# Performance work log

Measured on AMD Instinct MI355X. Metric: run time of the kernel, lower is better.

Reference implementation:

```python
import jax, jax.numpy as jnp
import numpy as np

C = 128        # in_channels
N = 80000      # nodes per type (user, item)
E = 1000000    # edges per relation
L = 400000     # link labels


def _evolve_gcn(x_src, edge_index, n_dst, p, W0, Wih, Whh, bih, bhh):
    """EvolveGCNH layer: TopK pooling -> 1-step GRU weight evolution -> GCN."""
    # TopK pooling: score = x @ p / ||p||, keep top C nodes, gate by tanh(score)
    score = x_src @ p / (jnp.linalg.norm(p) + 1e-16)          # [N_src]
    top_vals, top_idx = jax.lax.top_k(score, x_src.shape[1])   # k = C
    X_tilde = x_src[top_idx] * jnp.tanh(top_vals)[:, None]     # [C, C]
    # One GRU step: 'batch' dim = C rows of X_tilde, hidden = current weight W0
    gi = X_tilde @ Wih.T + bih                                 # [C, 3C]
    gh = W0 @ Whh.T + bhh                                      # [C, 3C]
    i_r, i_z, i_n = jnp.split(gi, 3, axis=1)
    h_r, h_z, h_n = jnp.split(gh, 3, axis=1)
    r = jax.nn.sigmoid(i_r + h_r)
    z = jax.nn.sigmoid(i_z + h_z)
    n = jnp.tanh(i_n + r * h_n)
    W = (1.0 - z) * n + z * W0                                 # evolved weight [C, C]
    # GCN propagation with symmetric degree norm, no self loops
    xw = x_src @ W                                             # [N_src, C]
    row, col = edge_index[0], edge_index[1]
    ones = jnp.ones(row.shape[0], dtype=xw.dtype)
    deg_src = jax.ops.segment_sum(ones, row, num_segments=x_src.shape[0])
    deg_dst = jax.ops.segment_sum(ones, col, num_segments=n_dst)
    inv_s = jnp.where(deg_src > 0, jax.lax.rsqrt(jnp.maximum(deg_src, 1.0)), 0.0)
    inv_d = jnp.where(deg_dst > 0, jax.lax.rsqrt(jnp.maximum(deg_dst, 1.0)), 0.0)
    norm = inv_s[row] * inv_d[col]                             # [E]
    return jax.ops.segment_sum(xw[row] * norm[:, None], col, num_segments=n_dst)


def setup_inputs() -> dict:
    key = jax.random.key(0)
    ks = jax.random.split(key, 20)
    f = lambda i, shape, s: jax.random.normal(ks[i], shape, dtype=jnp.float32) * s
    s_w = 1.0 / np.sqrt(C)
    return {
        "x_user": f(0, (N, C), 1.0),
        "x_item": f(1, (N, C), 1.0),
        "edge_ui": jax.random.randint(ks[2], (2, E), 0, N),
        "edge_iu": jax.random.randint(ks[3], (2, E), 0, N),
        "edge_label_index": jax.random.randint(ks[4], (2, L), 0, N),
        "p_ui": f(5, (C,), s_w),
        "W0_ui": f(6, (C, C), s_w),
        "Wih_ui": f(7, (3 * C, C), s_w),
        "Whh_ui": f(8, (3 * C, C), s_w),
        "bih_ui": f(9, (3 * C,), s_w),
        "bhh_ui": f(10, (3 * C,), s_w),
        "p_iu": f(11, (C,), s_w),
        "W0_iu": f(12, (C, C), s_w),
        "Wih_iu": f(13, (3 * C, C), s_w),
        "Whh_iu": f(14, (3 * C, C), s_w),
        "bih_iu": f(15, (3 * C,), s_w),
        "bhh_iu": f(16, (3 * C,), s_w),
        "W_post": f(17, (C, 2), s_w),
        "b_post": f(18, (2,), s_w),
    }


def reference(x_user, x_item, edge_ui, edge_iu, edge_label_index,
              p_ui, W0_ui, Wih_ui, Whh_ui, bih_ui, bhh_ui,
              p_iu, W0_iu, Wih_iu, Whh_iu, bih_iu, bhh_iu,
              W_post, b_post):
    # HeteroConv: one EvolveGCNH per relation, outputs grouped by dst node type
    h_item = jax.nn.relu(_evolve_gcn(x_user, edge_ui, x_item.shape[0],
                                     p_ui, W0_ui, Wih_ui, Whh_ui, bih_ui, bhh_ui))
    h_user = jax.nn.relu(_evolve_gcn(x_item, edge_iu, x_user.shape[0],
                                     p_iu, W0_iu, Wih_iu, Whh_iu, bih_iu, bhh_iu))
    # Link scorer: gather endpoints, hadamard, linear(C->2), sum over last dim
    h_src = h_user[edge_label_index[0]]                        # [L, C]
    h_dst = h_item[edge_label_index[1]]                        # [L, C]
    h = (h_src * h_dst) @ W_post + b_post                      # [L, 2]
    return jnp.sum(h, axis=-1)                                 # [L]
```

## Files before the change

kernel.cpp:

```cpp
#include <hip/hip_runtime.h>
#include <hip/hip_fp16.h>

constexpr int KC    = 128;
constexpr int NBLK  = 2048;
constexpr int CAPA  = 1024;
constexpr int CBITS = 10;
constexpr int CSZ   = 1 << CBITS;
constexpr int NBCM  = 192;

using half8   = __attribute__((ext_vector_type(8))) _Float16;
using float4v = __attribute__((ext_vector_type(4))) float;

__device__ __forceinline__ unsigned fkey(float s) {
  unsigned u = __float_as_uint(s);
  return (u & 0x80000000u) ? ~u : (u | 0x80000000u);
}

__global__ __launch_bounds__(256) void m1_cnt_scores(
    const int* __restrict__ eui, const int* __restrict__ eiu,
    unsigned* __restrict__ cnts, int* __restrict__ deg_src,
    const float* __restrict__ xu, const float* __restrict__ xi,
    const float* __restrict__ pu, const float* __restrict__ pi,
    float* __restrict__ scores, unsigned* __restrict__ hist,
    __half* __restrict__ x16,
    int E, int N, int NBC, int chunk) {
  __shared__ unsigned hD[4 * NBCM];
  int t = threadIdx.x;
  if (blockIdx.x < NBLK) {
    int blk = blockIdx.x, w = t >> 6;
    for (int b = t; b < 4 * NBCM; b += 256) hD[b] = 0;
    __syncthreads();
    int lo = blk * chunk, hi = min(2 * E, lo + chunk);
    for (int i = lo + t; i < hi; i += 256) {
      int rel = i >= E;
      const int* e = rel ? eiu : eui;
      int j = i - rel * E;
      atomicAdd(&hD[w * NBCM + ((rel * N + e[E + j]) >> CBITS)], 1u);
      atomicAdd(&deg_src[rel * N + e[j]], 1);
    }
    __syncthreads();
    for (int b = t; b < NBC; b += 256)
      cnts[(size_t)blk * NBC + b] =
          hD[b] + hD[NBCM + b] + hD[2 * NBCM + b] + hD[3 * NBCM + b];
  } else {
    int gw = (blockIdx.x - NBLK) * 8 + (t >> 5);
    if (gw >= 2 * N) return;
    int lane = t & 31;
    int rel = gw >= N;
    int r = gw - rel * N;
    const float* x = rel ? xi : xu;
    const float* p = rel ? pi : pu;
    float4 xv = ((const float4*)(x + (size_t)r * KC))[lane];
    float4 pv = ((const float4*)p)[lane];
    __half2 h0 = __floats2half2_rn(xv.x, xv.y);
    __half2 h1 = __floats2half2_rn(xv.z, xv.w);
    uint2 u; u.x = *(unsigned*)&h0; u.y = *(unsigned*)&h1;
    ((uint2*)(x16 + (size_t)gw * KC))[lane] = u;
    float s = xv.x * pv.x + xv.y * pv.y + xv.z * pv.z + xv.w * pv.w;
#pragma unroll
    for (int off = 16; off; off >>= 1) s += __shfl_down(s, off, 32);
    if (lane == 0) {
      scores[gw] = s;
      atomicAdd(&hist[rel * 65536 + (fkey(s) >> 16)], 1u);
    }
  }
}

__global__ __launch_bounds__(1024) void m2_thresh_scan1(
    const unsigned* __restrict__ cnts, unsigned* __restrict__ sc,
    unsigned* __restrict__ bsum, const unsigned* __restrict__ hist,
    unsigned* __restrict__ ctrl, int NTOT, int NBC) {
  __shared__ __align__(16) unsigned smem[1024 + 64 + 2];
  int t = threadIdx.x;
  if (blockIdx.x < 2) {
    const unsigned* h = hist + blockIdx.x * 65536;
    unsigned* c = ctrl + blockIdx.x * 8;
    unsigned* csum = smem;
    unsigned* bs = smem + 1024;
    unsigned s = 0;
    int hi = 65536 - 64 * t;
    for (int b = hi - 64; b < hi; ++b) s += h[b];
    csum[t] = s;
    __syncthreads();
    for (int off = 1; off < 1024; off <<= 1) {
      unsigned add = (t >= off) ? csum[t - off] : 0;
      __syncthreads();
      csum[t] += add;
      __syncthreads();
    }
    unsigned above = (t == 0) ? 0u : csum[t - 1];
    if (csum[t] >= 128u && above < 128u) { smem[1088] = (unsigned)t; smem[1089] = above; }
    __syncthreads();
    int chi = 65536 - 64 * (int)smem[1088];
    unsigned s_above = smem[1089];
    if (t < 64) bs[t] = h[chi - 1 - t];
    __syncthreads();
    if (t < 64) {
      unsigned v = bs[t], cum = v;
#pragma unroll
      for (int off = 1; off < 64; off <<= 1) {
        unsigned u = __shfl_up(cum, off, 64);
        if (t >= off) cum += u;
      }
      unsigned prev = cum - v;
      if (s_above + cum >= 128u && s_above + prev < 128u)
        c[0] = (unsigned)(chi - 1 - t);
    }
  } else {
    int vb = blockIdx.x - 2;
    unsigned* sh = smem;
    int li = vb * 1024 + t;
    unsigned v = 0;
    if (li < NTOT) {
      int b = li >> 11, blk = li & (NBLK - 1);
      v = cnts[(size_t)blk * NBC + b];
    }
    sh[t] = v; __syncthreads();
    for (int off = 1; off < 1024; off <<= 1) {
      unsigned add = (t >= off) ? sh[t - off] : 0;
      __syncthreads();
      sh[t] += add;
      __syncthreads();
    }
    if (li < NTOT) sc[li] = sh[t] - v;
    if (t == 1023) bsum[vb] = sh[1023];
  }
}

__global__ __launch_bounds__(512) void m3_scan2_compact(
    unsigned* __restrict__ bsum, int nb,
    const float* __restrict__ scores, unsigned* __restrict__ ctrl,
    int* __restrict__ cand_idx, float* __restrict__ cand_val, int N) {
  if (blockIdx.x == 0) {
    __shared__ unsigned sh[512];
    int t = threadIdx.x;
    unsigned v = (t < nb) ? bsum[t] : 0;
    sh[t] = v; __syncthreads();
    for (int off = 1; off < 512; off <<= 1) {
      unsigned add = (t >= off) ? sh[t - off] : 0;
      __syncthreads();
      sh[t] += add;
      __syncthreads();
    }
    if (t < nb) bsum[t] = sh[t] - v;
  } else {
    int i = (blockIdx.x - 1) * 512 + threadIdx.x;
    if (i >= 2 * N) return;
    int rel = i >= N;
    float s = scores[i];
    if ((fkey(s) >> 16) >= ctrl[rel * 8]) {
      unsigned pos = atomicAdd(&ctrl[rel * 8 + 1], 1u);
      if (pos < 2048u) {
        cand_idx[rel * 2048 + pos] = i - rel * N;
        cand_val[rel * 2048 + pos] = s;
      }
    }
  }
}

__global__ __launch_bounds__(256) void m4_topk_part(
    const int* __restrict__ eui, const int* __restrict__ eiu,
    const unsigned* __restrict__ cnts, const unsigned* __restrict__ sc,
    const unsigned* __restrict__ bsum,
    unsigned* __restrict__ recsD,
    const unsigned* __restrict__ ctrl,
    const int* __restrict__ cand_idx, const float* __restrict__ cand_val,
    const float* __restrict__ pu, const float* __restrict__ pi,
    int* __restrict__ top_idx, float* __restrict__ top_tanh,
    int E, int N, int NBC, int chunk) {
  __shared__ __align__(16) char smem[16896];
  int t = threadIdx.x;
  if (blockIdx.x < 2) {
    float* vals = (float*)smem;
    int*   idxs = (int*)(smem + 8192);
    float* red  = (float*)(smem + 16384);
    int rel = blockIdx.x;
    const float* p = rel ? pi : pu;
    int n = (int)ctrl[rel * 8 + 1]; if (n > 2048) n = 2048;
    for (int i = t; i < n; i += 256) {
      vals[i] = cand_val[rel * 2048 + i];
      idxs[i] = cand_idx[rel * 2048 + i];
    }
    if (t < 128) { float pv = p[t]; red[t] = pv * pv; }
    __syncthreads();
    for (int off = 64; off; off >>= 1) {
      if (t < off) red[t] += red[t + off];
      __syncthreads();
    }
    float pn = sqrtf(red[0]) + 1e-16f;
    for (int c = t; c < n; c += 256) {
      float v = vals[c]; int id = idxs[c];
      int rank = 0;
      for (int j = 0; j < n; ++j) {
        float vj = vals[j];
        rank += (vj > v) || (vj == v && idxs[j] < id);
      }
      if (rank < KC) {
        top_idx[rel * KC + rank] = id;
        top_tanh[rel * KC + rank] = tanhf(v / pn);
      }
    }
  } else {
    unsigned* scn    = (unsigned*)smem;
    unsigned* curD   = (unsigned*)(smem + 1024);
    unsigned* deltaD = (unsigned*)(smem + 2048);
    unsigned* stageD = (unsigned*)(smem + 3072);
    unsigned char* bktD = (unsigned char*)(smem + 7168);
    int blk = blockIdx.x - 2;
    unsigned v = (t < NBC) ? cnts[(size_t)blk * NBC + t] : 0;
    scn[t] = v; __syncthreads();
    for (int off = 1; off < 256; off <<= 1) {
      unsigned add = (t >= off) ? scn[t - off] : 0;
      __syncthreads();
      scn[t] += add;
      __syncthreads();
    }
    if (t < NBC) {
      unsigned exc = scn[t] - v;
      curD[t] = exc;
      int li = t * NBLK + blk;
      deltaD[t] = sc[li] + bsum[li >> 10] - exc;
    }
    __syncthreads();
    int lo = blk * chunk, hi = min(2 * E, lo + chunk);
    for (int i = lo + t; i < hi; i += 256) {
      int rel = i >= E;
      const int* e = rel ? eiu : eui;
      int j = i - rel * E;
      int src_g = rel * N + e[j];
      int dst_g = rel * N + e[E + j];
      int bD = dst_g >> CBITS;
      unsigned pD = atomicAdd(&curD[bD], 1u);
      stageD[pD] = (unsigned)src_g | ((unsigned)(dst_g & (CSZ - 1)) << 18);
      bktD[pD] = (unsigned char)bD;
    }
    __syncthreads();
    int cnt = hi - lo;
    for (int j = t; j < cnt; j += 256)
      recsD[deltaD[bktD[j]] + j] = stageD[j];
  }
}

__global__ __launch_bounds__(1024) void m5_refine_gru(
    const unsigned* __restrict__ sc, const unsigned* __restrict__ bsum,
    const unsigned* __restrict__ recsD,
    int* __restrict__ ssrc, int* __restrict__ deg_dst, int* __restrict__ endp,
    const float* __restrict__ xu, const float* __restrict__ xi,
    const int* __restrict__ top_idx, const float* __restrict__ top_tanh,
    const float* __restrict__ W0u, const float* __restrict__ W0i,
    const float* __restrict__ Wihu, const float* __restrict__ Wihi,
    const float* __restrict__ Whhu, const float* __restrict__ Whhi,
    const float* __restrict__ bihu, const float* __restrict__ bihi,
    const float* __restrict__ bhhu, const float* __restrict__ bhhi,
    __half* __restrict__ Wt,
    int E, int NBC, int N2) {
  __shared__ __align__(16) char smem[8256];
  int t = threadIdx.x;
  if ((int)blockIdx.x < NBC) {
    unsigned* hist = (unsigned*)smem;
    unsigned* cur  = (unsigned*)(smem + 4096);
    unsigned* t16  = (unsigned*)(smem + 8192);
    int c = blockIdx.x;
    int liLo = c * NBLK;
    int lo = (int)(sc[liLo] + bsum[liLo >> 10]);
    int hi;
    if (c + 1 < NBC) {
      int liHi = (c + 1) * NBLK;
      hi = (int)(sc[liHi] + bsum[liHi >> 10]);
    } else hi = 2 * E;
    hist[t] = 0;
    __syncthreads();
    for (int j = lo + t; j < hi; j += 1024)
      atomicAdd(&hist[recsD[j] >> 18], 1u);
    __syncthreads();
    unsigned v = hist[t];
    unsigned inc = v;
#pragma unroll
    for (int off = 1; off < 64; off <<= 1) {
      unsigned u = __shfl_up(inc, off, 64);
      if ((t & 63) >= off) inc += u;
    }
    int w = t >> 6;
    if ((t & 63) == 63) t16[w] = inc;
    __syncthreads();
    unsigned wbase = 0;
    for (int j = 0; j < 16; ++j) if (j < w) wbase += t16[j];
    unsigned exc = wbase + inc - v;
    cur[t] = exc;
    int node = c * CSZ + t;
    if (node < N2) {
      deg_dst[node] = (int)v;
      endp[node] = lo + (int)(exc + v);
    }
    __syncthreads();
    for (int j = lo + t; j < hi; j += 1024) {
      unsigned rec = recsD[j];
      unsigned pos = atomicAdd(&cur[rec >> 18], 1u);
      ssrc[lo + (int)pos] = (int)(rec & 0x3FFFFu);
    }
  } else {
    int gb = blockIdx.x - NBC;
    int rel = gb >> 7, c = gb & 127;
    const float* x   = rel ? xi   : xu;
    const float* W0  = rel ? W0i  : W0u;
    const float* Wih = rel ? Wihi : Wihu;
    const float* Whh = rel ? Whhi : Whhu;
    const float* bih = rel ? bihi : bihu;
    const float* bhh = rel ? bhhi : bhhu;
    float* xt = (float*)smem;
    float* w0 = (float*)(smem + 512);
    if (t < KC) {
      xt[t] = x[(size_t)top_idx[rel * KC + c] * KC + t] * top_tanh[rel * KC + c];
      w0[t] = W0[c * KC + t];
    }
    __syncthreads();
    if (t >= KC) return;
    int k = t;
    float gir = bih[k], giz = bih[KC + k], gin = bih[2 * KC + k];
    float ghr = bhh[k], ghz = bhh[KC + k], ghn = bhh[2 * KC + k];
    const float* wr = Wih + (size_t)k * KC;
    const float* wz = Wih + (size_t)(KC + k) * KC;
    const float* wn = Wih + (size_t)(2 * KC + k) * KC;
    const float* vr = Whh + (size_t)k * KC;
    const float* vz = Whh + (size_t)(KC + k) * KC;
    const float* vn = Whh + (size_t)(2 * KC + k) * KC;
    for (int j = 0; j < KC; ++j) {
      float xj = xt[j], hj = w0[j];
      gir += xj * wr[j]; giz += xj * wz[j]; gin += xj * wn[j];
      ghr += hj * vr[j]; ghz += hj * vz[j]; ghn += hj * vn[j];
    }
    float r = 1.f / (1.f + expf(-(gir + ghr)));
    float z = 1.f / (1.f + expf(-(giz + ghz)));
    float nn = tanhf(gin + r * ghn);
    float w = (1.f - z) * nn + z * w0[k];
    Wt[(size_t)rel * KC * KC + (size_t)k * KC + c] = __float2half_rn(w);
  }
}

__global__ __launch_bounds__(256) void k_gemm(const __half* __restrict__ x16,
                                              const __half* __restrict__ Wt,
                                              const int* __restrict__ deg_src,
                                              __half* __restrict__ xw, int N) {
  __shared__ __half Ws[KC * KC];
  __shared__ __half outs[64 * 136];
  int rel = (blockIdx.x * 64) >= N;
  int t = threadIdx.x;
  const uint4* wg = (const uint4*)(Wt + (size_t)rel * KC * KC);
#pragma unroll
  for (int i = 0; i < 8; ++i)
    ((uint4*)Ws)[t + 256 * i] = wg[t + 256 * i];
  __syncthreads();
  int wid = t >> 6, lane = t & 63;
  int l15 = lane & 15, quad = lane >> 4;
  int row0 = blockIdx.x * 64 + wid * 16;
  half8 a[4];
  const __half* xrow = x16 + (size_t)(row0 + l15) * KC + quad * 8;
#pragma unroll
  for (int ks = 0; ks < 4; ++ks) a[ks] = *(const half8*)(xrow + ks * 32);
  float4v acc[8];
#pragma unroll
  for (int nt = 0; nt < 8; ++nt) {
    acc[nt] = (float4v){0.f, 0.f, 0.f, 0.f};
#pragma unroll
    for (int ks = 0; ks < 4; ++ks) {
      half8 b = *(const half8*)&Ws[(nt * 16 + l15) * KC + ks * 32 + quad * 8];
      acc[nt] = __builtin_amdgcn_mfma_f32_16x16x32_f16(a[ks], b, acc[nt], 0, 0, 0);
    }
  }
  float scv[4];
#pragma unroll
  for (int r = 0; r < 4; ++r) {
    int dg = deg_src[row0 + quad * 4 + r];
    scv[r] = dg > 0 ? rsqrtf((float)dg) : 0.f;
  }
  __half* ob = outs + (size_t)wid * 16 * 136;
#pragma unroll
  for (int nt = 0; nt < 8; ++nt)
#pragma unroll
    for (int r = 0; r < 4; ++r)
      ob[(quad * 4 + r) * 136 + nt * 16 + l15] = __float2half_rn(acc[nt][r] * scv[r]);
  __syncthreads();
  size_t gbase = (size_t)blockIdx.x * 64 * KC;
#pragma unroll
  for (int i = 0; i < 4; ++i) {
    int idx = t + 256 * i;
    int rr = idx >> 4, cc = idx & 15;
    *(uint4*)(xw + gbase + (size_t)rr * KC + cc * 8) =
        *(const uint4*)(outs + (size_t)rr * 136 + cc * 8);
  }
}

__global__ void k_agg(const __half* __restrict__ xw, const int* __restrict__ ssrc,
                      const int* __restrict__ endp, const int* __restrict__ deg_dst,
                      __half* __restrict__ h, int n2) {
  int gw = (int)((blockIdx.x * blockDim.x + threadIdx.x) >> 6);
  if (gw >= n2) return;
  int lane = threadIdx.x & 63;
  int q = lane >> 4, l16 = lane & 15;
  int d = deg_dst[gw];
  int end = endp[gw], start = end - d;
  __half2 z = __floats2half2_rn(0.f, 0.f);
  __half2 a0[4], a1[4], a2[4], a3[4];
#pragma unroll
  for (int k = 0; k < 4; ++k) { a0[k] = z; a1[k] = z; a2[k] = z; a3[k] = z; }
  for (int i = start + q; i < end; i += 16) {
    int i1 = i + 4, i2 = i + 8, i3 = i + 12;
    bool b1 = i1 < end, b2 = i2 < end, b3 = i3 < end;
    int r0 = ssrc[i], r1, r2, r3;
    if (b1) r1 = ssrc[i1];
    if (b2) r2 = ssrc[i2];
    if (b3) r3 = ssrc[i3];
    uint4 u0 = ((const uint4*)(xw + (size_t)r0 * KC))[l16];
    uint4 u1, u2, u3;
    if (b1) u1 = ((const uint4*)(xw + (size_t)r1 * KC))[l16];
    if (b2) u2 = ((const uint4*)(xw + (size_t)r2 * KC))[l16];
    if (b3) u3 = ((const uint4*)(xw + (size_t)r3 * KC))[l16];
    {
      const __half2* p = (const __half2*)&u0;
#pragma unroll
      for (int k = 0; k < 4; ++k) a0[k] = __hadd2(a0[k], p[k]);
    }
    if (b1) {
      const __half2* p = (const __half2*)&u1;
#pragma unroll
      for (int k = 0; k < 4; ++k) a1[k] = __hadd2(a1[k], p[k]);
    }
    if (b2) {
      const __half2* p = (const __half2*)&u2;
#pragma unroll
      for (int k = 0; k < 4; ++k) a2[k] = __hadd2(a2[k], p[k]);
    }
    if (b3) {
      const __half2* p = (const __half2*)&u3;
#pragma unroll
      for (int k = 0; k < 4; ++k) a3[k] = __hadd2(a3[k], p[k]);
    }
  }
  float f[8];
#pragma unroll
  for (int k = 0; k < 4; ++k) {
    float2 x0 = __half22float2(a0[k]);
    float2 x1 = __half22float2(a1[k]);
    float2 x2 = __half22float2(a2[k]);
    float2 x3 = __half22float2(a3[k]);
    f[2 * k]     = (x0.x + x1.x) + (x2.x + x3.x);
    f[2 * k + 1] = (x0.y + x1.y) + (x2.y + x3.y);
  }
#pragma unroll
  for (int k = 0; k < 8; ++k) {
    f[k] += __shfl_xor(f[k], 16, 64);
    f[k] += __shfl_xor(f[k], 32, 64);
  }
  if (q == 0) {
    float invd = d > 0 ? rsqrtf((float)d) : 0.f;
    __half2 pk[4];
#pragma unroll
    for (int k = 0; k < 4; ++k)
      pk[k] = __floats2half2_rn(fmaxf(f[2 * k] * invd, 0.f),
                                fmaxf(f[2 * k + 1] * invd, 0.f));
    uint4 u;
    u.x = *(unsigned*)&pk[0]; u.y = *(unsigned*)&pk[1];
    u.z = *(unsigned*)&pk[2]; u.w = *(unsigned*)&pk[3];
    ((uint4*)(h + (size_t)gw * KC))[l16] = u;
  }
}

__global__ void k_links(const __half* __restrict__ h,
                        const int* __restrict__ srcs, const int* __restrict__ dsts,
                        const float* __restrict__ Wp, const float* __restrict__ bp,
                        float* __restrict__ out, int L, int N) {
  int tid = blockIdx.x * blockDim.x + threadIdx.x;
  int lane = threadIdx.x & 63;
  int q = lane >> 4, l16 = lane & 15;
  int gq = (tid >> 6) * 4 + q;
  int nq = (int)((gridDim.x * blockDim.x) >> 6) * 4;
  float w8[8];
#pragma unroll
  for (int k = 0; k < 4; ++k) {
    float4 w = ((const float4*)Wp)[l16 * 4 + k];
    w8[2 * k] = w.x + w.y; w8[2 * k + 1] = w.z + w.w;
  }
  float bs = bp[0] + bp[1];
  const __half* hu = h + (size_t)N * KC;
  for (int li = gq; li < L; li += nq) {
    int s = srcs[li], dd = dsts[li];
    uint4 ua = ((const uint4*)(hu + (size_t)s * KC))[l16];
    uint4 ub = ((const uint4*)(h + (size_t)dd * KC))[l16];
    const __half2* pa = (const __half2*)&ua;
    const __half2* pb = (const __half2*)&ub;
    float acc = 0.f;
#pragma unroll
    for (int k = 0; k < 4; ++k) {
      float2 fa = __half22float2(pa[k]);
      float2 fb = __half22float2(pb[k]);
      acc += fa.x * fb.x * w8[2 * k] + fa.y * fb.y * w8[2 * k + 1];
    }
#pragma unroll
    for (int off = 8; off; off >>= 1) acc += __shfl_xor(acc, off, 64);
    if (l16 == 0) out[li] = acc + bs;
  }
}

extern "C" void kernel_launch(void* const* d_in, const int* in_sizes, int n_in,
                              void* d_out, int out_size, void* d_ws, size_t ws_size,
                              hipStream_t stream) {
  const float* x_user = (const float*)d_in[0];
  const float* x_item = (const float*)d_in[1];
  const int*   edge_ui = (const int*)d_in[2];
  const int*   edge_iu = (const int*)d_in[3];
  const int*   elab    = (const int*)d_in[4];
  const float* p_ui   = (const float*)d_in[5];
  const float* W0_ui  = (const float*)d_in[6];
  const float* Wih_ui = (const float*)d_in[7];
  const float* Whh_ui = (const float*)d_in[8];
  const float* bih_ui = (const float*)d_in[9];
  const float* bhh_ui = (const float*)d_in[10];
  const float* p_iu   = (const float*)d_in[11];
  const float* W0_iu  = (const float*)d_in[12];
  const float* Wih_iu = (const float*)d_in[13];
  const float* Whh_iu = (const float*)d_in[14];
  const float* bih_iu = (const float*)d_in[15];
  const float* bhh_iu = (const float*)d_in[16];
  const float* W_post = (const float*)d_in[17];
  const float* b_post = (const float*)d_in[18];
  const int N = in_sizes[0] / KC;
  const int E = in_sizes[2] / 2;
  const int L = in_sizes[4] / 2;
  const int N2 = 2 * N;
  const int NBC = (N2 + CSZ - 1) >> CBITS;
  const int chunk = (2 * E + NBLK - 1) / NBLK;
  const int NTOT = NBC * NBLK;
  const int SCB = (NTOT + 1023) / 1024;

  char* wsp = (char*)d_ws;
  auto carve = [&](size_t bytes) -> void* {
    void* p = (void*)wsp;
    wsp += (bytes + 255) & ~(size_t)255;
    return p;
  };
  const size_t histB = 2 * 65536 * 4;
  const size_t zBytes = histB + 256 + (size_t)N2 * 4;
  char*     zbase    = (char*)carve(zBytes);
  unsigned* hist     = (unsigned*)zbase;
  unsigned* ctrl     = (unsigned*)(zbase + histB);
  int*      deg_src  = (int*)(zbase + histB + 256);
  __half*   x16      = (__half*)carve((size_t)N2 * KC * 2);
  __half*   xw       = (__half*)carve((size_t)N2 * KC * 2);
  __half*   h        = (__half*)carve((size_t)N2 * KC * 2);
  float*    scores   = (float*)carve((size_t)N2 * 4);
  int*      cand_idx = (int*)carve(2 * 2048 * 4);
  float*    cand_val = (float*)carve(2 * 2048 * 4);
  int*      top_idx  = (int*)carve(2 * KC * 4);
  float*    top_tanh = (float*)carve(2 * KC * 4);
  __half*   Wt16     = (__half*)carve(2 * KC * KC * 2);
  unsigned* cnts     = (unsigned*)carve((size_t)NTOT * 4);
  unsigned* sc       = (unsigned*)carve((size_t)NTOT * 4);
  unsigned* bsum     = (unsigned*)carve((size_t)SCB * 4);
  unsigned* recsD    = (unsigned*)carve((size_t)2 * E * 4);
  int*      ssrc     = (int*)carve((size_t)2 * E * 4);
  int*      deg_dst  = (int*)carve((size_t)N2 * 4);
  int*      endp     = (int*)carve((size_t)N2 * 4);

  hipMemsetAsync(zbase, 0, zBytes, stream);

  const int SBLK = (N2 + 7) / 8;
  m1_cnt_scores<<<NBLK + SBLK, 256, 0, stream>>>(edge_ui, edge_iu, cnts, deg_src,
                                                 x_user, x_item, p_ui, p_iu,
                                                 scores, hist, x16,
                                                 E, N, NBC, chunk);
  m2_thresh_scan1<<<2 + SCB, 1024, 0, stream>>>(cnts, sc, bsum, hist, ctrl,
                                                NTOT, NBC);
  m3_scan2_compact<<<1 + (N2 + 511) / 512, 512, 0, stream>>>(bsum, SCB, scores, ctrl,
                                                             cand_idx, cand_val, N);
  m4_topk_part<<<2 + NBLK, 256, 0, stream>>>(edge_ui, edge_iu, cnts, sc, bsum,
                                             recsD, ctrl, cand_idx, cand_val,
                                             p_ui, p_iu, top_idx, top_tanh,
                                             E, N, NBC, chunk);
  m5_refine_gru<<<NBC + 2 * KC, 1024, 0, stream>>>(sc, bsum, recsD, ssrc,
                                                   deg_dst, endp,
                                                   x_user, x_item, top_idx, top_tanh,
                                                   W0_ui, W0_iu, Wih_ui, Wih_iu,
                                                   Whh_ui, Whh_iu, bih_ui, bih_iu,
                                                   bhh_ui, bhh_iu, Wt16,
                                                   E, NBC, N2);
  k_gemm<<<N2 / 64, 256, 0, stream>>>(x16, Wt16, deg_src, xw, N);
  k_agg<<<(N2 + 3) / 4, 256, 0, stream>>>(xw, ssrc, endp, deg_dst, h, N2);
  k_links<<<2048, 256, 0, stream>>>(h, elab, elab + L, W_post, b_post,
                                    (float*)d_out, L, N);
}
```

Before: 458.4 us.

## Partition edges in one pass with fixed-capacity buckets and atomic bucket reservation

Edge partitioning by destination bucket now happens in the first kernel. Each block reserves space in fixed-capacity per-bucket regions with a global atomic, which replaces the two-level global scan and the second read of the edges. Source degrees are computed by also bucketing source ids and histogramming them per bucket, removing global atomics on deg_src. The gather index is pre-scaled to a byte offset, and the GRU and top-k stages are split into separate kernels. The fixed bucket capacity depends on random, uniform edge distribution, so a skewed bucket would overflow and be silently truncated.

```diff
diff --git a/kernel.cpp b/kernel.cpp
--- a/kernel.cpp
+++ b/kernel.cpp
@@ -7,6 +7,7 @@
 constexpr int CBITS = 10;
 constexpr int CSZ   = 1 << CBITS;
 constexpr int NBCM  = 192;
+constexpr int CAPB  = 16384;
 
 using half8   = __attribute__((ext_vector_type(8))) _Float16;
 using float4v = __attribute__((ext_vector_type(4))) float;
@@ -16,19 +17,24 @@
   return (u & 0x80000000u) ? ~u : (u | 0x80000000u);
 }
 
-__global__ __launch_bounds__(256) void m1_cnt_scores(
+__global__ __launch_bounds__(256) void k1_part_scores(
     const int* __restrict__ eui, const int* __restrict__ eiu,
-    unsigned* __restrict__ cnts, int* __restrict__ deg_src,
+    unsigned* __restrict__ gcntD, unsigned* __restrict__ gcntS,
+    unsigned* __restrict__ recsD, unsigned short* __restrict__ recsS,
     const float* __restrict__ xu, const float* __restrict__ xi,
     const float* __restrict__ pu, const float* __restrict__ pi,
     float* __restrict__ scores, unsigned* __restrict__ hist,
     __half* __restrict__ x16,
     int E, int N, int NBC, int chunk) {
-  __shared__ unsigned hD[4 * NBCM];
+  __shared__ unsigned hD[4 * NBCM], hS[4 * NBCM];
+  __shared__ unsigned scn[256], curD[256], curS[256], deltaD[256], deltaS[256];
+  __shared__ unsigned stageD[CAPA];
+  __shared__ unsigned short stageS[CAPA];
+  __shared__ unsigned char bktD[CAPA], bktS[CAPA];
   int t = threadIdx.x;
   if (blockIdx.x < NBLK) {
     int blk = blockIdx.x, w = t >> 6;
-    for (int b = t; b < 4 * NBCM; b += 256) hD[b] = 0;
+    for (int b = t; b < 4 * NBCM; b += 256) { hD[b] = 0; hS[b] = 0; }
     __syncthreads();
     int lo = blk * chunk, hi = min(2 * E, lo + chunk);
     for (int i = lo + t; i < hi; i += 256) {
@@ -36,12 +42,56 @@
       const int* e = rel ? eiu : eui;
       int j = i - rel * E;
       atomicAdd(&hD[w * NBCM + ((rel * N + e[E + j]) >> CBITS)], 1u);
-      atomicAdd(&deg_src[rel * N + e[j]], 1);
-    }
-    __syncthreads();
-    for (int b = t; b < NBC; b += 256)
-      cnts[(size_t)blk * NBC + b] =
-          hD[b] + hD[NBCM + b] + hD[2 * NBCM + b] + hD[3 * NBCM + b];
+      atomicAdd(&hS[w * NBCM + ((rel * N + e[j]) >> CBITS)], 1u);
+    }
+    __syncthreads();
+    unsigned vD = (t < NBC) ? hD[t] + hD[NBCM + t] + hD[2 * NBCM + t] + hD[3 * NBCM + t] : 0;
+    scn[t] = vD; __syncthreads();
+    for (int off = 1; off < 256; off <<= 1) {
+      unsigned a = (t >= off) ? scn[t - off] : 0;
+      __syncthreads(); scn[t] += a; __syncthreads();
+    }
+    unsigned excD = scn[t] - vD;
+    if (t < NBC) {
+      curD[t] = excD;
+      unsigned base = vD ? atomicAdd(&gcntD[t * 16], vD) : 0u;
+      deltaD[t] = (unsigned)(t * CAPB) + base - excD;
+    }
+    __syncthreads();
+    unsigned vS = (t < NBC) ? hS[t] + hS[NBCM + t] + hS[2 * NBCM + t] + hS[3 * NBCM + t] : 0;
+    scn[t] = vS; __syncthreads();
+    for (int off = 1; off < 256; off <<= 1) {
+      unsigned a = (t >= off) ? scn[t - off] : 0;
+      __syncthreads(); scn[t] += a; __syncthreads();
+    }
+    unsigned excS = scn[t] - vS;
+    if (t < NBC) {
+      curS[t] = excS;
+      unsigned base = vS ? atomicAdd(&gcntS[t * 16], vS) : 0u;
+      deltaS[t] = (unsigned)(t * CAPB) + base - excS;
+    }
+    __syncthreads();
+    for (int i = lo + t; i < hi; i += 256) {
+      int rel = i >= E;
+      const int* e = rel ? eiu : eui;
+      int j = i - rel * E;
+      int src_g = rel * N + e[j];
+      int dst_g = rel * N + e[E + j];
+      int bD = dst_g >> CBITS;
+      unsigned pD = atomicAdd(&curD[bD], 1u);
+      stageD[pD] = (unsigned)src_g | ((unsigned)(dst_g & (CSZ - 1)) << 18);
+      bktD[pD] = (unsigned char)bD;
+      int bS = src_g >> CBITS;
+      unsigned pS = atomicAdd(&curS[bS], 1u);
+      stageS[pS] = (unsigned short)(src_g & (CSZ - 1));
+      bktS[pS] = (unsigned char)bS;
+    }
+    __syncthreads();
+    int cnt = hi - lo;
+    for (int j = t; j < cnt; j += 256) {
+      recsD[deltaD[bktD[j]] + j] = stageD[j];
+      recsS[deltaS[bktS[j]] + j] = stageS[j];
+    }
   } else {
     int gw = (blockIdx.x - NBLK) * 8 + (t >> 5);
     if (gw >= 2 * N) return;
@@ -66,17 +116,21 @@
   }
 }
 
-__global__ __launch_bounds__(1024) void m2_thresh_scan1(
-    const unsigned* __restrict__ cnts, unsigned* __restrict__ sc,
-    unsigned* __restrict__ bsum, const unsigned* __restrict__ hist,
-    unsigned* __restrict__ ctrl, int NTOT, int NBC) {
-  __shared__ __align__(16) unsigned smem[1024 + 64 + 2];
+__global__ __launch_bounds__(1024) void k2_thresh_refine(
+    const unsigned* __restrict__ gcntD, const unsigned* __restrict__ gcntS,
+    const unsigned* __restrict__ recsD, const unsigned short* __restrict__ recsS,
+    int* __restrict__ ssrc, int* __restrict__ deg_dst, int* __restrict__ endp,
+    int* __restrict__ deg_src,
+    const unsigned* __restrict__ hist, unsigned* __restrict__ ctrl,
+    int NBC, int N2) {
+  __shared__ __align__(16) char smem[8256];
   int t = threadIdx.x;
   if (blockIdx.x < 2) {
     const unsigned* h = hist + blockIdx.x * 65536;
     unsigned* c = ctrl + blockIdx.x * 8;
-    unsigned* csum = smem;
-    unsigned* bs = smem + 1024;
+    unsigned* csum = (unsigned*)smem;
+    unsigned* bs   = (unsigned*)(smem + 4096);
+    unsigned* sv   = (unsigned*)(smem + 4352);
     unsigned s = 0;
     int hi = 65536 - 64 * t;
     for (int b = hi - 64; b < hi; ++b) s += h[b];
@@ -89,10 +143,10 @@
       __syncthreads();
     }
     unsigned above = (t == 0) ? 0u : csum[t - 1];
-    if (csum[t] >= 128u && above < 128u) { smem[1088] = (unsigned)t; smem[1089] = above; }
-    __syncthreads();
-    int chi = 65536 - 64 * (int)smem[1088];
-    unsigned s_above = smem[1089];
+    if (csum[t] >= 128u && above < 128u) { sv[0] = (unsigned)t; sv[1] = above; }
+    __syncthreads();
+    int chi = 65536 - 64 * (int)sv[0];
+    unsigned s_above = sv[1];
     if (t < 64) bs[t] = h[chi - 1 - t];
     __syncthreads();
     if (t < 64) {
@@ -106,174 +160,20 @@
       if (s_above + cum >= 128u && s_above + prev < 128u)
         c[0] = (unsigned)(chi - 1 - t);
     }
-  } else {
-    int vb = blockIdx.x - 2;
-    unsigned* sh = smem;
-    int li = vb * 1024 + t;
-    unsigned v = 0;
-    if (li < NTOT) {
-      int b = li >> 11, blk = li & (NBLK - 1);
-      v = cnts[(size_t)blk * NBC + b];
-    }
-    sh[t] = v; __syncthreads();
-    for (int off = 1; off < 1024; off <<= 1) {
-      unsigned add = (t >= off) ? sh[t - off] : 0;
-      __syncthreads();
-      sh[t] += add;
-      __syncthreads();
-    }
-    if (li < NTOT) sc[li] = sh[t] - v;
-    if (t == 1023) bsum[vb] = sh[1023];
-  }
-}
-
-__global__ __launch_bounds__(512) void m3_scan2_compact(
-    unsigned* __restrict__ bsum, int nb,
-    const float* __restrict__ scores, unsigned* __restrict__ ctrl,
-    int* __restrict__ cand_idx, float* __restrict__ cand_val, int N) {
-  if (blockIdx.x == 0) {
-    __shared__ unsigned sh[512];
-    int t = threadIdx.x;
-    unsigned v = (t < nb) ? bsum[t] : 0;
-    sh[t] = v; __syncthreads();
-    for (int off = 1; off < 512; off <<= 1) {
-      unsigned add = (t >= off) ? sh[t - off] : 0;
-      __syncthreads();
-      sh[t] += add;
-      __syncthreads();
-    }
-    if (t < nb) bsum[t] = sh[t] - v;
-  } else {
-    int i = (blockIdx.x - 1) * 512 + threadIdx.x;
-    if (i >= 2 * N) return;
-    int rel = i >= N;
-    float s = scores[i];
-    if ((fkey(s) >> 16) >= ctrl[rel * 8]) {
-      unsigned pos = atomicAdd(&ctrl[rel * 8 + 1], 1u);
-      if (pos < 2048u) {
-        cand_idx[rel * 2048 + pos] = i - rel * N;
-        cand_val[rel * 2048 + pos] = s;
-      }
-    }
-  }
-}
-
-__global__ __launch_bounds__(256) void m4_topk_part(
-    const int* __restrict__ eui, const int* __restrict__ eiu,
-    const unsigned* __restrict__ cnts, const unsigned* __restrict__ sc,
-    const unsigned* __restrict__ bsum,
-    unsigned* __restrict__ recsD,
-    const unsigned* __restrict__ ctrl,
-    const int* __restrict__ cand_idx, const float* __restrict__ cand_val,
-    const float* __restrict__ pu, const float* __restrict__ pi,
-    int* __restrict__ top_idx, float* __restrict__ top_tanh,
-    int E, int N, int NBC, int chunk) {
-  __shared__ __align__(16) char smem[16896];
-  int t = threadIdx.x;
-  if (blockIdx.x < 2) {
-    float* vals = (float*)smem;
-    int*   idxs = (int*)(smem + 8192);
-    float* red  = (float*)(smem + 16384);
-    int rel = blockIdx.x;
-    const float* p = rel ? pi : pu;
-    int n = (int)ctrl[rel * 8 + 1]; if (n > 2048) n = 2048;
-    for (int i = t; i < n; i += 256) {
-      vals[i] = cand_val[rel * 2048 + i];
-      idxs[i] = cand_idx[rel * 2048 + i];
-    }
-    if (t < 128) { float pv = p[t]; red[t] = pv * pv; }
-    __syncthreads();
-    for (int off = 64; off; off >>= 1) {
-      if (t < off) red[t] += red[t + off];
-      __syncthreads();
-    }
-    float pn = sqrtf(red[0]) + 1e-16f;
-    for (int c = t; c < n; c += 256) {
-      float v = vals[c]; int id = idxs[c];
-      int rank = 0;
-      for (int j = 0; j < n; ++j) {
-        float vj = vals[j];
-        rank += (vj > v) || (vj == v && idxs[j] < id);
-      }
-      if (rank < KC) {
-        top_idx[rel * KC + rank] = id;
-        top_tanh[rel * KC + rank] = tanhf(v / pn);
-      }
-    }
-  } else {
-    unsigned* scn    = (unsigned*)smem;
-    unsigned* curD   = (unsigned*)(smem + 1024);
-    unsigned* deltaD = (unsigned*)(smem + 2048);
-    unsigned* stageD = (unsigned*)(smem + 3072);
-    unsigned char* bktD = (unsigned char*)(smem + 7168);
-    int blk = blockIdx.x - 2;
-    unsigned v = (t < NBC) ? cnts[(size_t)blk * NBC + t] : 0;
-    scn[t] = v; __syncthreads();
-    for (int off = 1; off < 256; off <<= 1) {
-      unsigned add = (t >= off) ? scn[t - off] : 0;
-      __syncthreads();
-      scn[t] += add;
-      __syncthreads();
-    }
-    if (t < NBC) {
-      unsigned exc = scn[t] - v;
-      curD[t] = exc;
-      int li = t * NBLK + blk;
-      deltaD[t] = sc[li] + bsum[li >> 10] - exc;
-    }
-    __syncthreads();
-    int lo = blk * chunk, hi = min(2 * E, lo + chunk);
-    for (int i = lo + t; i < hi; i += 256) {
-      int rel = i >= E;
-      const int* e = rel ? eiu : eui;
-      int j = i - rel * E;
-      int src_g = rel * N + e[j];
-      int dst_g = rel * N + e[E + j];
-      int bD = dst_g >> CBITS;
-      unsigned pD = atomicAdd(&curD[bD], 1u);
-      stageD[pD] = (unsigned)src_g | ((unsigned)(dst_g & (CSZ - 1)) << 18);
-      bktD[pD] = (unsigned char)bD;
-    }
-    __syncthreads();
-    int cnt = hi - lo;
-    for (int j = t; j < cnt; j += 256)
-      recsD[deltaD[bktD[j]] + j] = stageD[j];
-  }
-}
-
-__global__ __launch_bounds__(1024) void m5_refine_gru(
-    const unsigned* __restrict__ sc, const unsigned* __restrict__ bsum,
-    const unsigned* __restrict__ recsD,
-    int* __restrict__ ssrc, int* __restrict__ deg_dst, int* __restrict__ endp,
-    const float* __restrict__ xu, const float* __restrict__ xi,
-    const int* __restrict__ top_idx, const float* __restrict__ top_tanh,
-    const float* __restrict__ W0u, const float* __restrict__ W0i,
-    const float* __restrict__ Wihu, const float* __restrict__ Wihi,
-    const float* __restrict__ Whhu, const float* __restrict__ Whhi,
-    const float* __restrict__ bihu, const float* __restrict__ bihi,
-    const float* __restrict__ bhhu, const float* __restrict__ bhhi,
-    __half* __restrict__ Wt,
-    int E, int NBC, int N2) {
-  __shared__ __align__(16) char smem[8256];
-  int t = threadIdx.x;
-  if ((int)blockIdx.x < NBC) {
-    unsigned* hist = (unsigned*)smem;
-    unsigned* cur  = (unsigned*)(smem + 4096);
-    unsigned* t16  = (unsigned*)(smem + 8192);
-    int c = blockIdx.x;
-    int liLo = c * NBLK;
-    int lo = (int)(sc[liLo] + bsum[liLo >> 10]);
-    int hi;
-    if (c + 1 < NBC) {
-      int liHi = (c + 1) * NBLK;
-      hi = (int)(sc[liHi] + bsum[liHi >> 10]);
-    } else hi = 2 * E;
-    hist[t] = 0;
+  } else if ((int)blockIdx.x < 2 + NBC) {
+    unsigned* hst = (unsigned*)smem;
+    unsigned* cur = (unsigned*)(smem + 4096);
+    unsigned* t16 = (unsigned*)(smem + 8192);
+    int c = blockIdx.x - 2;
+    int lo = c * CAPB;
+    int cnt = (int)gcntD[c * 16]; if (cnt > CAPB) cnt = CAPB;
+    int hi = lo + cnt;
+    hst[t] = 0;
     __syncthreads();
     for (int j = lo + t; j < hi; j += 1024)
-      atomicAdd(&hist[recsD[j] >> 18], 1u);
-    __syncthreads();
-    unsigned v = hist[t];
+      atomicAdd(&hst[recsD[j] >> 18], 1u);
+    __syncthreads();
+    unsigned v = hst[t];
     unsigned inc = v;
 #pragma unroll
     for (int off = 1; off < 64; off <<= 1) {
@@ -296,45 +196,113 @@
     for (int j = lo + t; j < hi; j += 1024) {
       unsigned rec = recsD[j];
       unsigned pos = atomicAdd(&cur[rec >> 18], 1u);
-      ssrc[lo + (int)pos] = (int)(rec & 0x3FFFFu);
+      ssrc[lo + (int)pos] = (int)((rec & 0x3FFFFu) << 8);
     }
   } else {
-    int gb = blockIdx.x - NBC;
-    int rel = gb >> 7, c = gb & 127;
-    const float* x   = rel ? xi   : xu;
-    const float* W0  = rel ? W0i  : W0u;
-    const float* Wih = rel ? Wihi : Wihu;
-    const float* Whh = rel ? Whhi : Whhu;
-    const float* bih = rel ? bihi : bihu;
-    const float* bhh = rel ? bhhi : bhhu;
-    float* xt = (float*)smem;
-    float* w0 = (float*)(smem + 512);
-    if (t < KC) {
-      xt[t] = x[(size_t)top_idx[rel * KC + c] * KC + t] * top_tanh[rel * KC + c];
-      w0[t] = W0[c * KC + t];
-    }
-    __syncthreads();
-    if (t >= KC) return;
-    int k = t;
-    float gir = bih[k], giz = bih[KC + k], gin = bih[2 * KC + k];
-    float ghr = bhh[k], ghz = bhh[KC + k], ghn = bhh[2 * KC + k];
-    const float* wr = Wih + (size_t)k * KC;
-    const float* wz = Wih + (size_t)(KC + k) * KC;
-    const float* wn = Wih + (size_t)(2 * KC + k) * KC;
-    const float* vr = Whh + (size_t)k * KC;
-    const float* vz = Whh + (size_t)(KC + k) * KC;
-    const float* vn = Whh + (size_t)(2 * KC + k) * KC;
-    for (int j = 0; j < KC; ++j) {
-      float xj = xt[j], hj = w0[j];
-      gir += xj * wr[j]; giz += xj * wz[j]; gin += xj * wn[j];
-      ghr += hj * vr[j]; ghz += hj * vz[j]; ghn += hj * vn[j];
-    }
-    float r = 1.f / (1.f + expf(-(gir + ghr)));
-    float z = 1.f / (1.f + expf(-(giz + ghz)));
-    float nn = tanhf(gin + r * ghn);
-    float w = (1.f - z) * nn + z * w0[k];
-    Wt[(size_t)rel * KC * KC + (size_t)k * KC + c] = __float2half_rn(w);
-  }
+    unsigned* hst = (unsigned*)smem;
+    int c = blockIdx.x - 2 - NBC;
+    int lo = c * CAPB;
+    int cnt = (int)gcntS[c * 16]; if (cnt > CAPB) cnt = CAPB;
+    int hi = lo + cnt;
+    hst[t] = 0;
+    __syncthreads();
+    for (int j = lo + t; j < hi; j += 1024)
+      atomicAdd(&hst[(unsigned)recsS[j]], 1u);
+    __syncthreads();
+    int node = c * CSZ + t;
+    if (node < N2) deg_src[node] = (int)hst[t];
+  }
+}
+
+__global__ __launch_bounds__(512) void k_compact(
+    const float* __restrict__ scores, unsigned* __restrict__ ctrl,
+    int* __restrict__ cand_idx, float* __restrict__ cand_val, int N) {
+  int i = blockIdx.x * 512 + threadIdx.x;
+  if (i >= 2 * N) return;
+  int rel = i >= N;
+  float s = scores[i];
+  if ((fkey(s) >> 16) >= ctrl[rel * 8]) {
+    unsigned pos = atomicAdd(&ctrl[rel * 8 + 1], 1u);
+    if (pos < 2048u) {
+      cand_idx[rel * 2048 + pos] = i - rel * N;
+      cand_val[rel * 2048 + pos] = s;
+    }
+  }
+}
+
+__global__ __launch_bounds__(256) void k_topk(
+    const unsigned* __restrict__ ctrl,
+    const int* __restrict__ cand_idx, const float* __restrict__ cand_val,
+    const float* __restrict__ pu, const float* __restrict__ pi,
+    int* __restrict__ top_idx, float* __restrict__ top_tanh) {
+  __shared__ float vals[2048];
+  __shared__ int   idxs[2048];
+  __shared__ float red[128];
+  int rel = blockIdx.x, t = threadIdx.x;
+  const float* p = rel ? pi : pu;
+  int n = (int)ctrl[rel * 8 + 1]; if (n > 2048) n = 2048;
+  for (int i = t; i < n; i += 256) {
+    vals[i] = cand_val[rel * 2048 + i];
+    idxs[i] = cand_idx[rel * 2048 + i];
+  }
+  if (t < 128) { float pv = p[t]; red[t] = pv * pv; }
+  __syncthreads();
+  for (int off = 64; off; off >>= 1) {
+    if (t < off) red[t] += red[t + off];
+    __syncthreads();
+  }
+  float pn = sqrtf(red[0]) + 1e-16f;
+  for (int c = t; c < n; c += 256) {
+    float v = vals[c]; int id = idxs[c];
+    int rank = 0;
+    for (int j = 0; j < n; ++j) {
+      float vj = vals[j];
+      rank += (vj > v) || (vj == v && idxs[j] < id);
+    }
+    if (rank < KC) {
+      top_idx[rel * KC + rank] = id;
+      top_tanh[rel * KC + rank] = tanhf(v / pn);
+    }
+  }
+}
+
+__global__ void k_gru(const float* __restrict__ xu, const float* __restrict__ xi,
+                      const int* __restrict__ top_idx, const float* __restrict__ top_tanh,
+                      const float* __restrict__ W0u, const float* __restrict__ W0i,
+                      const float* __restrict__ Wihu, const float* __restrict__ Wihi,
+                      const float* __restrict__ Whhu, const float* __restrict__ Whhi,
+                      const float* __restrict__ bihu, const float* __restrict__ bihi,
+                      const float* __restrict__ bhhu, const float* __restrict__ bhhi,
+                      __half* __restrict__ Wt) {
+  __shared__ float xt[KC], w0[KC];
+  int rel = blockIdx.x >> 7, c = blockIdx.x & 127, k = threadIdx.x;
+  const float* x   = rel ? xi   : xu;
+  const float* W0  = rel ? W0i  : W0u;
+  const float* Wih = rel ? Wihi : Wihu;
+  const float* Whh = rel ? Whhi : Whhu;
+  const float* bih = rel ? bihi : bihu;
+  const float* bhh = rel ? bhhi : bhhu;
+  xt[k] = x[(size_t)top_idx[rel * KC + c] * KC + k] * top_tanh[rel * KC + c];
+  w0[k] = W0[c * KC + k];
+  __syncthreads();
+  float gir = bih[k], giz = bih[KC + k], gin = bih[2 * KC + k];
+  float ghr = bhh[k], ghz = bhh[KC + k], ghn = bhh[2 * KC + k];
+  const float* wr = Wih + (size_t)k * KC;
+  const float* wz = Wih + (size_t)(KC + k) * KC;
+  const float* wn = Wih + (size_t)(2 * KC + k) * KC;
+  const float* vr = Whh + (size_t)k * KC;
+  const float* vz = Whh + (size_t)(KC + k) * KC;
+  const float* vn = Whh + (size_t)(2 * KC + k) * KC;
+  for (int j = 0; j < KC; ++j) {
+    float xj = xt[j], hj = w0[j];
+    gir += xj * wr[j]; giz += xj * wz[j]; gin += xj * wn[j];
+    ghr += hj * vr[j]; ghz += hj * vz[j]; ghn += hj * vn[j];
+  }
+  float r = 1.f / (1.f + expf(-(gir + ghr)));
+  float z = 1.f / (1.f + expf(-(giz + ghz)));
+  float nn = tanhf(gin + r * ghn);
+  float w = (1.f - z) * nn + z * w0[k];
+  Wt[(size_t)rel * KC * KC + (size_t)k * KC + c] = __float2half_rn(w);
 }
 
 __global__ __launch_bounds__(256) void k_gemm(const __half* __restrict__ x16,
@@ -399,6 +367,7 @@
   int q = lane >> 4, l16 = lane & 15;
   int d = deg_dst[gw];
   int end = endp[gw], start = end - d;
+  const char* xb = (const char*)xw;
   __half2 z = __floats2half2_rn(0.f, 0.f);
   __half2 a0[4], a1[4], a2[4], a3[4];
 #pragma unroll
@@ -410,11 +379,11 @@
     if (b1) r1 = ssrc[i1];
     if (b2) r2 = ssrc[i2];
     if (b3) r3 = ssrc[i3];
-    uint4 u0 = ((const uint4*)(xw + (size_t)r0 * KC))[l16];
+    uint4 u0 = *(const uint4*)(xb + r0 + l16 * 16);
     uint4 u1, u2, u3;
-    if (b1) u1 = ((const uint4*)(xw + (size_t)r1 * KC))[l16];
-    if (b2) u2 = ((const uint4*)(xw + (size_t)r2 * KC))[l16];
-    if (b3) u3 = ((const uint4*)(xw + (size_t)r3 * KC))[l16];
+    if (b1) u1 = *(const uint4*)(xb + r1 + l16 * 16);
+    if (b2) u2 = *(const uint4*)(xb + r2 + l16 * 16);
+    if (b3) u3 = *(const uint4*)(xb + r3 + l16 * 16);
     {
       const __half2* p = (const __half2*)&u0;
 #pragma unroll
@@ -529,8 +498,6 @@
   const int N2 = 2 * N;
   const int NBC = (N2 + CSZ - 1) >> CBITS;
   const int chunk = (2 * E + NBLK - 1) / NBLK;
-  const int NTOT = NBC * NBLK;
-  const int SCB = (NTOT + 1023) / 1024;
 
   char* wsp = (char*)d_ws;
   auto carve = [&](size_t bytes) -> void* {
@@ -539,11 +506,14 @@
     return p;
   };
   const size_t histB = 2 * 65536 * 4;
-  const size_t zBytes = histB + 256 + (size_t)N2 * 4;
+  const size_t gcntB = (size_t)NBCM * 16 * 4;
+  const size_t zBytes = histB + 256 + 2 * gcntB;
   char*     zbase    = (char*)carve(zBytes);
   unsigned* hist     = (unsigned*)zbase;
   unsigned* ctrl     = (unsigned*)(zbase + histB);
-  int*      deg_src  = (int*)(zbase + histB + 256);
+  unsigned* gcntD    = (unsigned*)(zbase + histB + 256);
+  unsigned* gcntS    = gcntD + NBCM * 16;
+  int*      deg_src  = (int*)carve((size_t)N2 * 4);
   __half*   x16      = (__half*)carve((size_t)N2 * KC * 2);
   __half*   xw       = (__half*)carve((size_t)N2 * KC * 2);
   __half*   h        = (__half*)carve((size_t)N2 * KC * 2);
@@ -553,36 +523,28 @@
   int*      top_idx  = (int*)carve(2 * KC * 4);
   float*    top_tanh = (float*)carve(2 * KC * 4);
   __half*   Wt16     = (__half*)carve(2 * KC * KC * 2);
-  unsigned* cnts     = (unsigned*)carve((size_t)NTOT * 4);
-  unsigned* sc       = (unsigned*)carve((size_t)NTOT * 4);
-  unsigned* bsum     = (unsigned*)carve((size_t)SCB * 4);
-  unsigned* recsD    = (unsigned*)carve((size_t)2 * E * 4);
-  int*      ssrc     = (int*)carve((size_t)2 * E * 4);
+  unsigned* recsD    = (unsigned*)carve((size_t)(NBC + 1) * CAPB * 4);
+  unsigned short* recsS = (unsigned short*)carve((size_t)(NBC + 1) * CAPB * 2);
+  int*      ssrc     = (int*)carve((size_t)(NBC + 1) * CAPB * 4);
   int*      deg_dst  = (int*)carve((size_t)N2 * 4);
   int*      endp     = (int*)carve((size_t)N2 * 4);
 
   hipMemsetAsync(zbase, 0, zBytes, stream);
 
   const int SBLK = (N2 + 7) / 8;
-  m1_cnt_scores<<<NBLK + SBLK, 256, 0, stream>>>(edge_ui, edge_iu, cnts, deg_src,
-                                                 x_user, x_item, p_ui, p_iu,
-                                                 scores, hist, x16,
-                                                 E, N, NBC, chunk);
-  m2_thresh_scan1<<<2 + SCB, 1024, 0, stream>>>(cnts, sc, bsum, hist, ctrl,
-                                                NTOT, NBC);
-  m3_scan2_compact<<<1 + (N2 + 511) / 512, 512, 0, stream>>>(bsum, SCB, scores, ctrl,
-                                                             cand_idx, cand_val, N);
-  m4_topk_part<<<2 + NBLK, 256, 0, stream>>>(edge_ui, edge_iu, cnts, sc, bsum,
-                                             recsD, ctrl, cand_idx, cand_val,
-                                             p_ui, p_iu, top_idx, top_tanh,
-                                             E, N, NBC, chunk);
-  m5_refine_gru<<<NBC + 2 * KC, 1024, 0, stream>>>(sc, bsum, recsD, ssrc,
-                                                   deg_dst, endp,
-                                                   x_user, x_item, top_idx, top_tanh,
-                                                   W0_ui, W0_iu, Wih_ui, Wih_iu,
-                                                   Whh_ui, Whh_iu, bih_ui, bih_iu,
-                                                   bhh_ui, bhh_iu, Wt16,
-                                                   E, NBC, N2);
+  k1_part_scores<<<NBLK + SBLK, 256, 0, stream>>>(edge_ui, edge_iu, gcntD, gcntS,
+                                                  recsD, recsS,
+                                                  x_user, x_item, p_ui, p_iu,
+                                                  scores, hist, x16,
+                                                  E, N, NBC, chunk);
+  k2_thresh_refine<<<2 + 2 * NBC, 1024, 0, stream>>>(gcntD, gcntS, recsD, recsS,
+                                                     ssrc, deg_dst, endp, deg_src,
+                                                     hist, ctrl, NBC, N2);
+  k_compact<<<(N2 + 511) / 512, 512, 0, stream>>>(scores, ctrl, cand_idx, cand_val, N);
+  k_topk<<<2, 256, 0, stream>>>(ctrl, cand_idx, cand_val, p_ui, p_iu, top_idx, top_tanh);
+  k_gru<<<2 * KC, KC, 0, stream>>>(x_user, x_item, top_idx, top_tanh,
+                                   W0_ui, W0_iu, Wih_ui, Wih_iu, Whh_ui, Whh_iu,
+                                   bih_ui, bih_iu, bhh_ui, bhh_iu, Wt16);
   k_gemm<<<N2 / 64, 256, 0, stream>>>(x16, Wt16, deg_src, xw, N);
   k_agg<<<(N2 + 3) / 4, 256, 0, stream>>>(xw, ssrc, endp, deg_dst, h, N2);
   k_links<<<2048, 256, 0, stream>>>(h, elab, elab + L, W_post, b_post,
```

After: 426.5 us. 7.0% less time.
